# Kernel tuning notes

Measured on AMD Instinct MI355X. Metric: run time of the kernel, lower is better.

The kernel has to match this reference:

```python
import jax, jax.numpy as jnp
import numpy as np

B, N, IN_DIM, HID, OUT_DIM = 8, 1024, 768, 128, 768
H1, H2, MHA_HEADS, C = 8, 1, 4, 32
ALPHA = 0.2
NEG = -9e15
LN_EPS = 1e-5


def _gat_layer(x, W, a1, a2, adj_mask):
    # x: [B,N,Fin], W: [H,Fin,Fout], a1/a2: [H,Fout], adj_mask: [B,N,N] bool
    h = jnp.einsum('bni,hio->bhno', x, W)                      # [B,H,N,F]
    s1 = jnp.einsum('bhno,ho->bhn', h, a1)                     # score for source node i
    s2 = jnp.einsum('bhno,ho->bhn', h, a2)                     # score for target node j
    e = jax.nn.leaky_relu(s1[:, :, :, None] + s2[:, :, None, :], negative_slope=ALPHA)
    e = jnp.where(adj_mask[:, None, :, :], e, NEG)
    attn = jax.nn.softmax(e, axis=-1)                          # [B,H,N,N]
    hp = jnp.einsum('bhnm,bhmo->bhno', attn, h)                # [B,H,N,F]
    b, nh, n, f = hp.shape
    return hp.transpose(0, 2, 1, 3).reshape(b, n, nh * f)      # concat heads -> [B,N,H*F]


def _mha(q, k, v, wq, bq, wk, bk, wv, bv, wo, bo, n_heads):
    # torch-style MultiheadAttention (eval, no dropout). q:[B,Lq,E] k,v:[B,Lk,E]
    b, lq, e = q.shape
    lk = k.shape[1]
    hd = e // n_heads
    Q = (q @ wq + bq).reshape(b, lq, n_heads, hd).transpose(0, 2, 1, 3)
    K = (k @ wk + bk).reshape(b, lk, n_heads, hd).transpose(0, 2, 1, 3)
    V = (v @ wv + bv).reshape(b, lk, n_heads, hd).transpose(0, 2, 1, 3)
    scores = jnp.einsum('bhqd,bhkd->bhqk', Q, K) / jnp.sqrt(jnp.float32(hd))
    attn = jax.nn.softmax(scores, axis=-1)
    out = jnp.einsum('bhqk,bhkd->bhqd', attn, V)
    out = out.transpose(0, 2, 1, 3).reshape(b, lq, e)
    return out @ wo + bo


def _layernorm(x, g, b):
    mu = jnp.mean(x, axis=-1, keepdims=True)
    var = jnp.var(x, axis=-1, keepdims=True)
    return (x - mu) * jax.lax.rsqrt(var + LN_EPS) * g + b


def setup_inputs() -> dict:
    key = jax.random.key(0)
    ks = jax.random.split(key, 24)
    s = lambda fan_in: 1.0 / np.sqrt(fan_in)
    inp = {
        'node_features': jax.random.normal(ks[0], (B, N, IN_DIM), jnp.float32),
        'adjacency': jax.random.randint(ks[1], (B, N, N), 0, 2, jnp.int32),
        'context_indices': jax.random.randint(ks[2], (B, C), 0, N, jnp.int32),
        # GAT layer 1: 8 heads, in=768 -> out=128 each
        'W1': jax.random.normal(ks[3], (H1, IN_DIM, HID), jnp.float32) * s(IN_DIM),
        'a1_1': jax.random.normal(ks[4], (H1, HID), jnp.float32) * s(2 * HID),
        'a2_1': jax.random.normal(ks[5], (H1, HID), jnp.float32) * s(2 * HID),
        # GAT layer 2: 1 head, in=1024 -> out=128
        'W2': jax.random.normal(ks[6], (H2, HID * H1, HID), jnp.float32) * s(HID * H1),
        'a1_2': jax.random.normal(ks[7], (H2, HID), jnp.float32) * s(2 * HID),
        'a2_2': jax.random.normal(ks[8], (H2, HID), jnp.float32) * s(2 * HID),
        # query MultiheadAttention (embed_dim=128, 4 heads)
        'wq': jax.random.normal(ks[9], (HID, HID), jnp.float32) * s(HID),
        'bq': jnp.zeros((HID,), jnp.float32),
        'wk': jax.random.normal(ks[10], (HID, HID), jnp.float32) * s(HID),
        'bk': jnp.zeros((HID,), jnp.float32),
        'wv': jax.random.normal(ks[11], (HID, HID), jnp.float32) * s(HID),
        'bv': jnp.zeros((HID,), jnp.float32),
        'wo': jax.random.normal(ks[12], (HID, HID), jnp.float32) * s(HID),
        'bo': jnp.zeros((HID,), jnp.float32),
        # projection MLP
        'p1_w': jax.random.normal(ks[13], (HID, HID), jnp.float32) * s(HID),
        'p1_b': jnp.zeros((HID,), jnp.float32),
        'ln_g': jnp.ones((HID,), jnp.float32),
        'ln_b': jnp.zeros((HID,), jnp.float32),
        'p2_w': jax.random.normal(ks[14], (HID, OUT_DIM), jnp.float32) * s(HID),
        'p2_b': jnp.zeros((OUT_DIM,), jnp.float32),
    }
    return inp


def reference(node_features, adjacency, context_indices,
              W1, a1_1, a2_1, W2, a1_2, a2_2,
              wq, bq, wk, bk, wv, bv, wo, bo,
              p1_w, p1_b, ln_g, ln_b, p2_w, p2_b):
    adj_mask = adjacency > 0
    h = jax.nn.elu(_gat_layer(node_features, W1, a1_1, a2_1, adj_mask))  # [B,N,1024]
    h = jax.nn.elu(_gat_layer(h, W2, a1_2, a2_2, adj_mask))              # [B,N,128]
    q = h[:, 0:1, :]                                                      # [B,1,E]
    ctx = jnp.take_along_axis(h, context_indices[:, :, None], axis=1)     # [B,C,E]
    pooled = _mha(q, ctx, ctx, wq, bq, wk, bk, wv, bv, wo, bo, MHA_HEADS)[:, 0, :]
    z = jax.nn.relu(_layernorm(pooled @ p1_w + p1_b, ln_g, ln_b))
    return z @ p2_w + p2_b                                                # [B,OUT_DIM]
```

## Files before the change

### kernel.cpp

```cpp
#include <hip/hip_runtime.h>
#include <hip/hip_bf16.h>

#define ALPHA 0.2f
#define LOG2E 1.4426950408889634f

using short8  = __attribute__((ext_vector_type(8))) short;
using short4v = __attribute__((ext_vector_type(4))) short;
using f32x4   = __attribute__((ext_vector_type(4))) float;
using int4v   = __attribute__((ext_vector_type(4))) int;

static __device__ __forceinline__ float b2f(short s) {
    union { float f; unsigned u; } v; v.u = ((unsigned)(unsigned short)s) << 16; return v.f;
}
static __device__ __forceinline__ short f2bf(float f) {
    __hip_bfloat16 h = __float2bfloat16(f);
    return *reinterpret_cast<short*>(&h);
}
static __device__ __forceinline__ float fexp2(float x) {
    return __builtin_amdgcn_exp2f(x);
}
static __device__ __forceinline__ void gload_lds16(const void* g, void* l) {
    __builtin_amdgcn_global_load_lds(
        (const __attribute__((address_space(1))) unsigned*)g,
        (__attribute__((address_space(3))) unsigned*)l, 16, 0, 0);
}

__global__ __launch_bounds__(256) void k_prep(
        const int* __restrict__ adj, unsigned* __restrict__ adjb,
        const float* __restrict__ x, short* __restrict__ xb,
        const float* __restrict__ W1, short* __restrict__ W1T,
        const float* __restrict__ W2, short* __restrict__ W2T) {
    int bid = blockIdx.x, t = threadIdx.x;
    if (bid < 32768) {
        int idx = bid * 256 + t;
        int lane = t & 63;
        unsigned long long m = __ballot(adj[idx] > 0);
        if ((lane & 31) == 0) adjb[idx >> 5] = (unsigned)(m >> (lane & 32));
    } else if (bid < 38912) {
        int idx = (bid - 32768) * 256 + t;
        f32x4 v = ((const f32x4*)x)[idx];
        short4v o;
        o[0] = f2bf(v[0]); o[1] = f2bf(v[1]); o[2] = f2bf(v[2]); o[3] = f2bf(v[3]);
        ((short4v*)xb)[idx] = o;
    } else if (bid < 41984) {
        int idx = (bid - 38912) * 256 + t;
        int n = idx / 768, k = idx - n * 768;
        int h = n >> 7, o = n & 127;
        W1T[idx] = f2bf(W1[(h * 768 + k) * 128 + o]);
    } else {
        int idx = (bid - 41984) * 256 + t;
        int n = idx >> 10, k = idx & 1023;
        W2T[idx] = f2bf(W2[k * 128 + n]);
    }
}

__global__ __launch_bounds__(256) void k_gemm_bt(
        const short* __restrict__ A, const short* __restrict__ Bt,
        short* __restrict__ Ct, int K, int Ncols,
        const float* __restrict__ a1, const float* __restrict__ a2,
        float* __restrict__ s1, float* __restrict__ s2) {
    int tid = threadIdx.x, wave = tid >> 6, lane = tid & 63;
    int lr = lane & 15, lg = lane >> 4;
    int flat = blockIdx.y * gridDim.x + blockIdx.x;
    int chunkw = (gridDim.x * gridDim.y) >> 3;
    int swz = (flat & 7) * chunkw + (flat >> 3);
    int bx = swz % gridDim.x, by = swz / gridDim.x;
    int m0 = bx * 128, n0 = by * 128;
    int wm = (wave >> 1) * 64, wn = (wave & 1) * 64;
    __shared__ short lsA[2][128 * 64], lsB[2][128 * 64];
    __shared__ float sred1[2][128], sred2[2][128];
    f32x4 acc[4][4];
#pragma unroll
    for (int i = 0; i < 4; i++)
#pragma unroll
        for (int j = 0; j < 4; j++) acc[i][j] = (f32x4){0.f, 0.f, 0.f, 0.f};

    auto stage = [&](int bufsel, int k0) {
#pragma unroll
        for (int s = 0; s < 4; s++) {
            int chunk = s * 256 + tid;
            int r = chunk >> 3, c = chunk & 7;
            int csrc = c ^ (r & 7);
            gload_lds16(A + (size_t)(m0 + r) * K + k0 + csrc * 8, &lsA[bufsel][chunk * 8]);
            gload_lds16(Bt + (size_t)(n0 + r) * K + k0 + csrc * 8, &lsB[bufsel][chunk * 8]);
        }
    };
    auto compute = [&](const short* la, const short* lb) {
#pragma unroll
        for (int kk = 0; kk < 2; kk++) {
            short8 a[4], bb[4];
#pragma unroll
            for (int f = 0; f < 4; f++) {
                int ra = wm + f * 16 + lr, rb = wn + f * 16 + lr;
                a[f]  = *(const short8*)(la + ra * 64 + (((kk * 4 + lg) ^ (ra & 7)) * 8));
                bb[f] = *(const short8*)(lb + rb * 64 + (((kk * 4 + lg) ^ (rb & 7)) * 8));
            }
#pragma unroll
            for (int fm = 0; fm < 4; fm++)
#pragma unroll
                for (int fn = 0; fn < 4; fn++)
                    acc[fm][fn] = __builtin_amdgcn_mfma_f32_16x16x32_bf16(a[fm], bb[fn], acc[fm][fn], 0, 0, 0);
        }
    };
    stage(0, 0);
    __syncthreads();
    for (int k2 = 0; k2 < K; k2 += 128) {
        stage(1, k2 + 64);
        compute(lsA[0], lsB[0]);
        __syncthreads();
        if (k2 + 128 < K) stage(0, k2 + 128);
        compute(lsA[1], lsB[1]);
        __syncthreads();
    }
    short* stg = &lsA[0][0];
#pragma unroll
    for (int fm = 0; fm < 4; fm++) {
#pragma unroll
        for (int fn = 0; fn < 4; fn++) {
            int nl = wn + fn * 16 + lr;
            int i4w = (wm + fm * 16 + lg * 4) >> 2;
            short4v st;
            st[0] = f2bf(acc[fm][fn][0]); st[1] = f2bf(acc[fm][fn][1]);
            st[2] = f2bf(acc[fm][fn][2]); st[3] = f2bf(acc[fm][fn][3]);
            *(short4v*)(stg + (nl * 32 + (i4w ^ (nl & 31))) * 4) = st;
        }
    }
    __syncthreads();
    size_t gbase = ((size_t)(m0 >> 10) * Ncols + n0) * 1024 + (m0 & 1023);
#pragma unroll
    for (int it = 0; it < 8; it++) {
        int idx8 = it * 256 + tid;
        int nl = idx8 >> 4, p = idx8 & 15;
        int i4a = 2 * p, i4b = 2 * p + 1;
        short4v lo = *(short4v*)(stg + (nl * 32 + (i4a ^ (nl & 31))) * 4);
        short4v hi = *(short4v*)(stg + (nl * 32 + (i4b ^ (nl & 31))) * 4);
        short8 v;
#pragma unroll
        for (int r = 0; r < 4; r++) { v[r] = lo[r]; v[r + 4] = hi[r]; }
        *(short8*)(Ct + gbase + (size_t)nl * 1024 + p * 8) = v;
    }
    if (a1 != nullptr) {
        int h = by;
        float av1[4], av2[4];
#pragma unroll
        for (int fn = 0; fn < 4; fn++) {
            int o = wn + fn * 16 + lr;
            av1[fn] = a1[h * 128 + o];
            av2[fn] = a2[h * 128 + o];
        }
        int wcol = wave & 1;
#pragma unroll
        for (int fm = 0; fm < 4; fm++)
#pragma unroll
            for (int r = 0; r < 4; r++) {
                float v1 = acc[fm][0][r] * av1[0] + acc[fm][1][r] * av1[1]
                         + acc[fm][2][r] * av1[2] + acc[fm][3][r] * av1[3];
                float v2 = acc[fm][0][r] * av2[0] + acc[fm][1][r] * av2[1]
                         + acc[fm][2][r] * av2[2] + acc[fm][3][r] * av2[3];
#pragma unroll
                for (int off = 1; off < 16; off <<= 1) {
                    v1 += __shfl_xor(v1, off);
                    v2 += __shfl_xor(v2, off);
                }
                if (lr == 0) {
                    int il = wm + fm * 16 + lg * 4 + r;
                    sred1[wcol][il] = v1;
                    sred2[wcol][il] = v2;
                }
            }
        __syncthreads();
        if (tid < 128) {
            int b = m0 >> 10;
            int irow = (b * 8 + h) * 1024 + (m0 & 1023) + tid;
            s1[irow] = (sred1[0][tid] + sred1[1][tid]) * LOG2E;
            s2[irow] = (sred2[0][tid] + sred2[1][tid]) * LOG2E;
        }
    }
}

__global__ __launch_bounds__(256) void k_gemm64(
        const short* __restrict__ A, const short* __restrict__ Bt,
        short* __restrict__ Ct, int K, int Ncols) {
    int tid = threadIdx.x, wave = tid >> 6, lane = tid & 63;
    int lr = lane & 15, lg = lane >> 4;
    int flat = blockIdx.y * gridDim.x + blockIdx.x;
    int chunkw = (gridDim.x * gridDim.y) >> 3;
    int swz = (flat & 7) * chunkw + (flat >> 3);
    int bx = swz % gridDim.x, by = swz / gridDim.x;
    int m0 = bx * 64, n0 = by * 64;
    int wm = (wave >> 1) * 32, wn = (wave & 1) * 32;
    __shared__ short lsA[2][64 * 32], lsB[2][64 * 32];
    f32x4 acc[2][2];
#pragma unroll
    for (int i = 0; i < 2; i++)
#pragma unroll
        for (int j = 0; j < 2; j++) acc[i][j] = (f32x4){0.f, 0.f, 0.f, 0.f};

    auto stage = [&](int bufsel, int k0) {
        int r = tid >> 2, c = tid & 3;
        int csrc = c ^ (r & 3);
        int base = (wave * 64) * 8;
        gload_lds16(A + (size_t)(m0 + r) * K + k0 + csrc * 8, &lsA[bufsel][base]);
        gload_lds16(Bt + (size_t)(n0 + r) * K + k0 + csrc * 8, &lsB[bufsel][base]);
    };
    stage(0, 0);
    __syncthreads();
    int buf = 0;
    for (int k0 = 0; k0 < K; k0 += 32) {
        if (k0 + 32 < K) stage(buf ^ 1, k0 + 32);
        short8 a[2], bb[2];
#pragma unroll
        for (int f = 0; f < 2; f++) {
            int ra = wm + f * 16 + lr, rb = wn + f * 16 + lr;
            a[f]  = *(const short8*)(&lsA[buf][ra * 32 + ((lg ^ (ra & 3)) * 8)]);
            bb[f] = *(const short8*)(&lsB[buf][rb * 32 + ((lg ^ (rb & 3)) * 8)]);
        }
#pragma unroll
        for (int fm = 0; fm < 2; fm++)
#pragma unroll
            for (int fn = 0; fn < 2; fn++)
                acc[fm][fn] = __builtin_amdgcn_mfma_f32_16x16x32_bf16(a[fm], bb[fn], acc[fm][fn], 0, 0, 0);
        __syncthreads();
        buf ^= 1;
    }
#pragma unroll
    for (int fm = 0; fm < 2; fm++) {
        int mb = m0 + wm + fm * 16 + lg * 4;
        size_t obase = ((size_t)(mb >> 10) * Ncols) * 1024 + (mb & 1023);
#pragma unroll
        for (int fn = 0; fn < 2; fn++) {
            int n = n0 + wn + fn * 16 + lr;
            short4v st;
            st[0] = f2bf(acc[fm][fn][0]); st[1] = f2bf(acc[fm][fn][1]);
            st[2] = f2bf(acc[fm][fn][2]); st[3] = f2bf(acc[fm][fn][3]);
            *(short4v*)(Ct + obase + (size_t)n * 1024) = st;
        }
    }
}

__global__ __launch_bounds__(256) void k_s12(
        const short* __restrict__ ht, const float* __restrict__ a1,
        const float* __restrict__ a2, float* __restrict__ s1,
        float* __restrict__ s2, int nh) {
    int bh = blockIdx.x;
    int h = bh % nh;
    int i4 = threadIdx.x * 4;
    const short* base = ht + (size_t)bh * 131072 + i4;
    f32x4 acc1 = {0.f, 0.f, 0.f, 0.f}, acc2 = {0.f, 0.f, 0.f, 0.f};
#pragma unroll 8
    for (int o = 0; o < 128; o++) {
        short4v v = *(const short4v*)(base + ((size_t)o << 10));
        float w1 = a1[h * 128 + o], w2 = a2[h * 128 + o];
#pragma unroll
        for (int r = 0; r < 4; r++) {
            float f = b2f(v[r]);
            acc1[r] += f * w1;
            acc2[r] += f * w2;
        }
    }
#pragma unroll
    for (int r = 0; r < 4; r++) { acc1[r] *= LOG2E; acc2[r] *= LOG2E; }
    *(f32x4*)(s1 + bh * 1024 + i4) = acc1;
    *(f32x4*)(s2 + bh * 1024 + i4) = acc2;
}

__global__ __launch_bounds__(512) void k_attn1(
        const short* __restrict__ ht, const unsigned* __restrict__ adjb,
        const float* __restrict__ s1, const float* __restrict__ s2,
        short* __restrict__ out) {
    int flat = blockIdx.y * 8 + blockIdx.x;
    int swz = (flat & 7) * 64 + (flat >> 3);
    int bh = swz >> 3, bxi = swz & 7;
    int b = bh >> 3, h = bh & 7;
    int tid = threadIdx.x, wave = tid >> 6, lane = tid & 63;
    int lr = lane & 15, lg = lane >> 4;
    int ic = bxi * 128 + wave * 16 + lr;
    int row = bh * 1024 + ic;
    float s1i = s1[row];
    const unsigned long long* abrow =
        (const unsigned long long*)(adjb + ((size_t)(b << 10) + ic) * 32);
    const float* s2r = s2 + bh * 1024;
    const short* hbase = ht + (size_t)bh * 131072;

    __shared__ short lsh[2][16384];
    __shared__ float ls2[1024];
    f32x4 acc[8];
#pragma unroll
    for (int f = 0; f < 8; f++) acc[f] = (f32x4){0.f, 0.f, 0.f, 0.f};
    f32x4 accs = (f32x4){0.f, 0.f, 0.f, 0.f};
    short8 ones8;
#pragma unroll
    for (int e = 0; e < 8; e++) ones8[e] = (short)0x3F80;

    auto stage = [&](int bufsel, int j0) {
#pragma unroll
        for (int s = 0; s < 4; s++) {
            int chunk = s * 512 + tid;
            int r = chunk >> 4, c = chunk & 15;
            int csrc = c ^ (r & 15);
            gload_lds16(hbase + (size_t)r * 1024 + j0 + csrc * 8,
                        &lsh[bufsel][chunk * 8]);
        }
    };
    auto compute = [&](const short* ls, int j0) {
        unsigned long long aw0 = abrow[j0 >> 6], aw1 = abrow[(j0 >> 6) + 1];
#pragma unroll
        for (int kk = 0; kk < 4; kk++) {
            int jb = j0 + kk * 32 + lg * 8;
            f32x4 t0 = *(const f32x4*)(&ls2[jb]);
            f32x4 t1 = *(const f32x4*)(&ls2[jb + 4]);
            unsigned long long aw = (kk < 2) ? aw0 : aw1;
            unsigned bits = (unsigned)(aw >> ((kk & 1) * 32 + lg * 8)) & 0xFFu;
            float pv[8];
#pragma unroll
            for (int e = 0; e < 8; e++) {
                float sv = e < 4 ? t0[e] : t1[e & 3];
                float ee = s1i + sv;
                ee = fmaxf(ee, ALPHA * ee);
                float p = fexp2(ee);
                pv[e] = ((bits >> e) & 1) ? p : 0.f;
            }
            int4v pw;
#pragma unroll
            for (int w = 0; w < 4; w++) {
                int d;
                asm("v_cvt_pk_bf16_f32 %0, %1, %2"
                    : "=v"(d) : "v"(pv[2 * w]), "v"(pv[2 * w + 1]));
                pw[w] = d;
            }
            short8 pb = __builtin_bit_cast(short8, pw);
            __builtin_amdgcn_s_setprio(1);
            accs = __builtin_amdgcn_mfma_f32_16x16x32_bf16(ones8, pb, accs, 0, 0, 0);
#pragma unroll
            for (int fm = 0; fm < 8; fm++) {
                int r = fm * 16 + lr;
                int ck = (kk * 4 + lg) ^ (r & 15);
                short8 af = *(const short8*)(ls + r * 128 + ck * 8);
                acc[fm] = __builtin_amdgcn_mfma_f32_16x16x32_bf16(af, pb, acc[fm], 0, 0, 0);
            }
            __builtin_amdgcn_s_setprio(0);
        }
    };

    if (wave < 4) {
        gload_lds16(s2r + (wave * 64 + lane) * 4, &ls2[wave * 256]);
    }
    stage(0, 0);
    __syncthreads();
    for (int t2 = 0; t2 < 1024; t2 += 256) {
        stage(1, t2 + 128);
        compute(lsh[0], t2);
        __syncthreads();
        if (t2 + 256 < 1024) stage(0, t2 + 256);
        compute(lsh[1], t2 + 128);
        __syncthreads();
    }
    float rdi = 1.f / accs[0];
    size_t orow = ((size_t)(b << 10) + ic) * 1024 + h * 128;
#pragma unroll
    for (int fm = 0; fm < 8; fm++) {
        int ob = (fm << 4) + lg * 4;
        short4v st;
#pragma unroll
        for (int r = 0; r < 4; r++) {
            float x = acc[fm][r] * rdi;
            x = x > 0.f ? x : expm1f(x);
            st[r] = f2bf(x);
        }
        *(short4v*)(out + orow + ob) = st;
    }
}

__global__ __launch_bounds__(256) void k_attn2g(
        const short* __restrict__ h2t, const unsigned* __restrict__ adjb,
        const float* __restrict__ s1, const float* __restrict__ s2,
        const int* __restrict__ cidx, float* __restrict__ ghat) {
    int tile = blockIdx.x;
    int b = blockIdx.y;
    int tid = threadIdx.x, wave = tid >> 6, lane = tid & 63;
    int lr = lane & 15, lg = lane >> 4;

    __shared__ int nodes[16];
    __shared__ float sps[4][16];
    __shared__ float sacc[4][16][129];

    if (tid < 16) {
        int pos = tile * 16 + tid;
        int nd = 0;
        if (pos >= 1 && pos <= 32) nd = cidx[b * 32 + pos - 1];
        nodes[tid] = nd;
    }
    __syncthreads();

    const float* s2r = s2 + b * 1024;
    int nd = nodes[lr];
    float s1i = s1[b * 1024 + nd];
    const unsigned long long* abrow =
        (const unsigned long long*)(adjb + ((size_t)(b << 10) + nd) * 32);
    const short* hb = h2t + (size_t)b * 131072;
    f32x4 acc[8];
#pragma unroll
    for (int f = 0; f < 8; f++) acc[f] = (f32x4){0.f, 0.f, 0.f, 0.f};
    float psum = 0.f;

    for (int j0 = wave * 256; j0 < wave * 256 + 256; j0 += 32) {
        int jb = j0 + lg * 8;
        f32x4 t0 = *(const f32x4*)(s2r + jb);
        f32x4 t1 = *(const f32x4*)(s2r + jb + 4);
        unsigned bits = (unsigned)(abrow[j0 >> 6] >> ((j0 & 32) + lg * 8)) & 0xFFu;
        short8 pb;
#pragma unroll
        for (int e = 0; e < 8; e++) {
            float sv = e < 4 ? t0[e] : t1[e & 3];
            float ee = s1i + sv;
            ee = fmaxf(ee, ALPHA * ee);
            float p = fexp2(ee);
            p = ((bits >> e) & 1) ? p : 0.f;
            psum += p;
            pb[e] = f2bf(p);
        }
#pragma unroll
        for (int fm = 0; fm < 8; fm++) {
            short8 af = *(const short8*)(hb + (size_t)(fm * 16 + lr) * 1024 + jb);
            acc[fm] = __builtin_amdgcn_mfma_f32_16x16x32_bf16(af, pb, acc[fm], 0, 0, 0);
        }
    }
    psum += __shfl_xor(psum, 16);
    psum += __shfl_xor(psum, 32);
    if (lg == 0) sps[wave][lr] = psum;
#pragma unroll
    for (int fm = 0; fm < 8; fm++)
#pragma unroll
        for (int r = 0; r < 4; r++)
            sacc[wave][lr][fm * 16 + lg * 4 + r] = acc[fm][r];
    __syncthreads();
    for (int e = tid; e < 2048; e += 256) {
        int li = e >> 7, o = e & 127;
        float sum = sps[0][li] + sps[1][li] + sps[2][li] + sps[3][li];
        float v = (sacc[0][li][o] + sacc[1][li][o] + sacc[2][li][o] + sacc[3][li][o]) / sum;
        v = v > 0.f ? v : expm1f(v);
        ghat[((size_t)b * 48 + tile * 16 + li) * 128 + o] = v;
    }
}

__global__ __launch_bounds__(256) void k_qkv(
        const float* __restrict__ ghat,
        const float* __restrict__ wk, const float* __restrict__ bk,
        const float* __restrict__ wvp, const float* __restrict__ bv,
        float* __restrict__ Kp, float* __restrict__ Vp) {
    int b = blockIdx.y, rg = blockIdx.x & 7, o0 = (blockIdx.x >> 3) * 64;
    int t = threadIdx.x, wvi = t >> 6, ln = t & 63;
    __shared__ float sx[4][128];
    __shared__ float sWk[128 * 64], sWv[128 * 64];

    if (wvi < 2) {
        int cb = wvi * 64;
        gload_lds16(ghat + ((size_t)b * 48 + 1 + rg * 4) * 128 + (size_t)(cb + ln) * 4,
                    (float*)sx + cb * 4);
    }
#pragma unroll
    for (int s = 0; s < 8; s++) {
        int cb = s * 256 + wvi * 64;
        int q = cb + ln, rw = q >> 4, c4 = q & 15;
        gload_lds16(wk  + (size_t)rw * 128 + o0 + c4 * 4, &sWk[cb * 4]);
        gload_lds16(wvp + (size_t)rw * 128 + o0 + c4 * 4, &sWv[cb * 4]);
    }
    __syncthreads();
    int o = o0 + ln;
    float ka = bk[o], va = bv[o];
#pragma unroll 32
    for (int c = 0; c < 128; c++) {
        float x = sx[wvi][c];
        ka += x * sWk[c * 64 + ln];
        va += x * sWv[c * 64 + ln];
    }
    int r = rg * 4 + wvi;
    Kp[((size_t)b * 32 + r) * 128 + o] = ka;
    Vp[((size_t)b * 32 + r) * 128 + o] = va;
}

__global__ __launch_bounds__(256) void k_tail(
        const float* __restrict__ ghat, const float* __restrict__ Kp,
        const float* __restrict__ Vp,
        const float* __restrict__ wq, const float* __restrict__ bq,
        const float* __restrict__ wo, const float* __restrict__ bo,
        const float* __restrict__ p1w, const float* __restrict__ p1b,
        const float* __restrict__ lng, const float* __restrict__ lnb,
        float* __restrict__ tvec) {
    int b = blockIdx.x, t = threadIdx.x;
    int wvi = t >> 6, ln = t & 63;
    __shared__ float sq[128], sQ[128], sK[32][128], sV[32][128];
    __shared__ float sP[4][33], sO[128], sT[128], sZ[128];
    __shared__ float sred[2];
    __shared__ float sW[128 * 128];

#pragma unroll
    for (int s = 0; s < 4; s++) {
        int cb = s * 256 + wvi * 64;
        gload_lds16(Kp + (size_t)b * 4096 + (size_t)(cb + ln) * 4, (float*)sK + cb * 4);
        gload_lds16(Vp + (size_t)b * 4096 + (size_t)(cb + ln) * 4, (float*)sV + cb * 4);
    }
#pragma unroll
    for (int s = 0; s < 16; s++) {
        int cb = s * 256 + wvi * 64;
        gload_lds16(wq + (size_t)(cb + ln) * 4, &sW[cb * 4]);
    }
    if (t < 128) sq[t] = ghat[(size_t)b * 48 * 128 + t];
    __syncthreads();
    if (t < 128) {
        float a0 = 0.f, a1 = 0.f, a2 = 0.f, a3 = 0.f;
#pragma unroll
        for (int c = 0; c < 128; c += 4) {
            a0 += sq[c]     * sW[c * 128 + t];
            a1 += sq[c + 1] * sW[(c + 1) * 128 + t];
            a2 += sq[c + 2] * sW[(c + 2) * 128 + t];
            a3 += sq[c + 3] * sW[(c + 3) * 128 + t];
        }
        sQ[t] = bq[t] + ((a0 + a1) + (a2 + a3));
    }
    __syncthreads();
#pragma unroll
    for (int s = 0; s < 16; s++) {
        int cb = s * 256 + wvi * 64;
        gload_lds16(wo + (size_t)(cb + ln) * 4, &sW[cb * 4]);
    }
    if (t < 128) {
        int hh = t >> 5, jj = t & 31;
        float s = 0.f;
#pragma unroll
        for (int d = 0; d < 32; d++) s += sQ[hh * 32 + d] * sK[jj][hh * 32 + d];
        s *= 0.17677669529663687f;
        float m = s;
#pragma unroll
        for (int off = 16; off > 0; off >>= 1) m = fmaxf(m, __shfl_xor(m, off, 32));
        float p = __expf(s - m);
        float sum = p;
#pragma unroll
        for (int off = 16; off > 0; off >>= 1) sum += __shfl_xor(sum, off, 32);
        sP[hh][jj] = p / sum;
    }
    __syncthreads();
    if (t < 128) {
        int hh = t >> 5;
        float s = 0.f;
#pragma unroll
        for (int jj = 0; jj < 32; jj++) s += sP[hh][jj] * sV[jj][t];
        sO[t] = s;
    }
    __syncthreads();
    if (t < 128) {
        float a0 = 0.f, a1 = 0.f, a2 = 0.f, a3 = 0.f;
#pragma unroll
        for (int c = 0; c < 128; c += 4) {
            a0 += sO[c]     * sW[c * 128 + t];
            a1 += sO[c + 1] * sW[(c + 1) * 128 + t];
            a2 += sO[c + 2] * sW[(c + 2) * 128 + t];
            a3 += sO[c + 3] * sW[(c + 3) * 128 + t];
        }
        sT[t] = bo[t] + ((a0 + a1) + (a2 + a3));
    }
    __syncthreads();
#pragma unroll
    for (int s = 0; s < 16; s++) {
        int cb = s * 256 + wvi * 64;
        gload_lds16(p1w + (size_t)(cb + ln) * 4, &sW[cb * 4]);
    }
    __syncthreads();
    if (t < 128) {
        float a0 = 0.f, a1 = 0.f, a2 = 0.f, a3 = 0.f;
#pragma unroll
        for (int c = 0; c < 128; c += 4) {
            a0 += sT[c]     * sW[c * 128 + t];
            a1 += sT[c + 1] * sW[(c + 1) * 128 + t];
            a2 += sT[c + 2] * sW[(c + 2) * 128 + t];
            a3 += sT[c + 3] * sW[(c + 3) * 128 + t];
        }
        sZ[t] = p1b[t] + ((a0 + a1) + (a2 + a3));
    }
    __syncthreads();
    if (t < 64) {
        float v = sZ[t] + sZ[t + 64];
#pragma unroll
        for (int off = 32; off > 0; off >>= 1) v += __shfl_xor(v, off);
        if (t == 0) sred[0] = v * (1.f / 128.f);
    }
    __syncthreads();
    float mu = sred[0];
    if (t < 64) {
        float d1 = sZ[t] - mu, d2 = sZ[t + 64] - mu;
        float v = d1 * d1 + d2 * d2;
#pragma unroll
        for (int off = 32; off > 0; off >>= 1) v += __shfl_xor(v, off);
        if (t == 0) sred[1] = v * (1.f / 128.f);
    }
    __syncthreads();
    float rstd = rsqrtf(sred[1] + 1e-5f);
    if (t < 128) {
        float z = (sZ[t] - mu) * rstd * lng[t] + lnb[t];
        tvec[b * 128 + t] = fmaxf(z, 0.f);
    }
}

__global__ __launch_bounds__(256) void k_p2(
        const float* __restrict__ tvec, const float* __restrict__ p2w,
        const float* __restrict__ p2b, float* __restrict__ out) {
    int jj0 = blockIdx.x * 128, b = blockIdx.y;
    int t = threadIdx.x, wvi = t >> 6, ln = t & 63;
    __shared__ float sT[128];
    __shared__ float sW[128 * 128];

#pragma unroll
    for (int s = 0; s < 16; s++) {
        int cb = s * 256 + wvi * 64;
        int q = cb + ln, c = q >> 5, c4 = q & 31;
        gload_lds16(p2w + (size_t)c * 768 + jj0 + c4 * 4, &sW[cb * 4]);
    }
    if (t < 128) sT[t] = tvec[b * 128 + t];
    __syncthreads();
    if (t < 128) {
        float a0 = 0.f, a1 = 0.f, a2 = 0.f, a3 = 0.f;
#pragma unroll
        for (int c = 0; c < 128; c += 4) {
            a0 += sT[c]     * sW[c * 128 + t];
            a1 += sT[c + 1] * sW[(c + 1) * 128 + t];
            a2 += sT[c + 2] * sW[(c + 2) * 128 + t];
            a3 += sT[c + 3] * sW[(c + 3) * 128 + t];
        }
        out[b * 768 + jj0 + t] = p2b[jj0 + t] + ((a0 + a1) + (a2 + a3));
    }
}

extern "C" void kernel_launch(void* const* d_in, const int* in_sizes, int n_in,
                              void* d_out, int out_size, void* d_ws, size_t ws_size,
                              hipStream_t stream) {
    const float* x   = (const float*)d_in[0];
    const int*  adj  = (const int*)d_in[1];
    const int*  cidx = (const int*)d_in[2];
    const float* W1  = (const float*)d_in[3];
    const float* a11 = (const float*)d_in[4];
    const float* a21 = (const float*)d_in[5];
    const float* W2  = (const float*)d_in[6];
    const float* a12 = (const float*)d_in[7];
    const float* a22 = (const float*)d_in[8];
    const float* wq = (const float*)d_in[9];  const float* bq = (const float*)d_in[10];
    const float* wk = (const float*)d_in[11]; const float* bk = (const float*)d_in[12];
    const float* wv = (const float*)d_in[13]; const float* bv = (const float*)d_in[14];
    const float* wo = (const float*)d_in[15]; const float* bo = (const float*)d_in[16];
    const float* p1w = (const float*)d_in[17]; const float* p1b = (const float*)d_in[18];
    const float* lng = (const float*)d_in[19]; const float* lnb = (const float*)d_in[20];
    const float* p2w = (const float*)d_in[21]; const float* p2b = (const float*)d_in[22];
    float* out = (float*)d_out;

    char* ws = (char*)d_ws;
    size_t off = 0;
    auto alloc = [&](size_t bytes) -> char* {
        char* p = ws + off;
        off = (off + bytes + 255) & ~(size_t)255;
        return p;
    };
    short* Xb   = (short*)alloc(8192ull * 768 * 2);
    short* W1T  = (short*)alloc(1024ull * 768 * 2);
    short* W2T  = (short*)alloc(128ull * 1024 * 2);
    unsigned* adjb = (unsigned*)alloc(8ull * 1024 * 32 * 4);
    short* h1t  = (short*)alloc(64ull * 128 * 1024 * 2);
    float* s1a  = (float*)alloc(64ull * 1024 * 4);
    float* s2a  = (float*)alloc(64ull * 1024 * 4);
    short* hcat = (short*)alloc(8192ull * 1024 * 2);
    short* h2t  = (short*)alloc(8ull * 128 * 1024 * 2);
    float* s1b  = (float*)alloc(8192ull * 4);
    float* s2b  = (float*)alloc(8192ull * 4);
    float* ghat = (float*)alloc(8ull * 48 * 128 * 4);
    float* Kp   = (float*)alloc(8ull * 32 * 128 * 4);
    float* Vp   = (float*)alloc(8ull * 32 * 128 * 4);
    float* tvec = (float*)alloc(8ull * 128 * 4);
    if (off > ws_size) return;

    k_prep<<<42496, 256, 0, stream>>>(adj, adjb, x, Xb, W1, W1T, W2, W2T);

    k_gemm_bt<<<dim3(64, 8), 256, 0, stream>>>(Xb, W1T, h1t, 768, 1024,
                                               a11, a21, s1a, s2a);
    k_attn1<<<dim3(8, 64), 512, 0, stream>>>(h1t, adjb, s1a, s2a, hcat);

    k_gemm64<<<dim3(128, 2), 256, 0, stream>>>(hcat, W2T, h2t, 1024, 128);
    k_s12<<<8, 256, 0, stream>>>(h2t, a12, a22, s1b, s2b, 1);
    k_attn2g<<<dim3(3, 8), 256, 0, stream>>>(h2t, adjb, s1b, s2b, cidx, ghat);

    k_qkv<<<dim3(16, 8), 256, 0, stream>>>(ghat, wk, bk, wv, bv, Kp, Vp);
    k_tail<<<8, 256, 0, stream>>>(ghat, Kp, Vp, wq, bq, wo, bo,
                                  p1w, p1b, lng, lnb, tvec);
    k_p2<<<dim3(6, 8), 256, 0, stream>>>(tvec, p2w, p2b, out);
}
```

Measured before the change: 148.1 us.

## Switch GAT layer-1 attention to 32x32x16 MFMA with 32 rows per wave

Rewrites k_attn1 so each wave handles 32 query rows using the 32x32x16 bf16 MFMA instead of 16 rows with 16x16x32, halving the block to 256 threads. The softmax denominator is now a per-lane running sum plus a cross-half shuffle, replacing the extra ones-vector MFMA. The goal is to halve the exp/leaky-relu work per P element and reduce LDS fragment reads per MFMA. In exchange each block uses fewer waves and larger accumulator registers, and has to issue twice as many staging loads per thread.

```diff
diff --git a/kernel.cpp b/kernel.cpp
--- a/kernel.cpp
+++ b/kernel.cpp
@@ -7,6 +7,7 @@
 using short8  = __attribute__((ext_vector_type(8))) short;
 using short4v = __attribute__((ext_vector_type(4))) short;
 using f32x4   = __attribute__((ext_vector_type(4))) float;
+using f32x16  = __attribute__((ext_vector_type(16))) float;
 using int4v   = __attribute__((ext_vector_type(4))) int;
 
 static __device__ __forceinline__ float b2f(short s) {
@@ -264,7 +265,7 @@
     *(f32x4*)(s2 + bh * 1024 + i4) = acc2;
 }
 
-__global__ __launch_bounds__(512) void k_attn1(
+__global__ __launch_bounds__(256) void k_attn1(
         const short* __restrict__ ht, const unsigned* __restrict__ adjb,
         const float* __restrict__ s1, const float* __restrict__ s2,
         short* __restrict__ out) {
@@ -273,8 +274,8 @@
     int bh = swz >> 3, bxi = swz & 7;
     int b = bh >> 3, h = bh & 7;
     int tid = threadIdx.x, wave = tid >> 6, lane = tid & 63;
-    int lr = lane & 15, lg = lane >> 4;
-    int ic = bxi * 128 + wave * 16 + lr;
+    int li = lane & 31, jh = lane >> 5;
+    int ic = bxi * 128 + wave * 32 + li;
     int row = bh * 1024 + ic;
     float s1i = s1[row];
     const unsigned long long* abrow =
@@ -284,18 +285,17 @@
 
     __shared__ short lsh[2][16384];
     __shared__ float ls2[1024];
-    f32x4 acc[8];
-#pragma unroll
-    for (int f = 0; f < 8; f++) acc[f] = (f32x4){0.f, 0.f, 0.f, 0.f};
-    f32x4 accs = (f32x4){0.f, 0.f, 0.f, 0.f};
-    short8 ones8;
-#pragma unroll
-    for (int e = 0; e < 8; e++) ones8[e] = (short)0x3F80;
+    f32x16 acc[4];
+#pragma unroll
+    for (int f = 0; f < 4; f++)
+#pragma unroll
+        for (int r = 0; r < 16; r++) acc[f][r] = 0.f;
+    float psum = 0.f;
 
     auto stage = [&](int bufsel, int j0) {
 #pragma unroll
-        for (int s = 0; s < 4; s++) {
-            int chunk = s * 512 + tid;
+        for (int s = 0; s < 8; s++) {
+            int chunk = s * 256 + tid;
             int r = chunk >> 4, c = chunk & 15;
             int csrc = c ^ (r & 15);
             gload_lds16(hbase + (size_t)r * 1024 + j0 + csrc * 8,
@@ -303,14 +303,13 @@
         }
     };
     auto compute = [&](const short* ls, int j0) {
-        unsigned long long aw0 = abrow[j0 >> 6], aw1 = abrow[(j0 >> 6) + 1];
-#pragma unroll
-        for (int kk = 0; kk < 4; kk++) {
-            int jb = j0 + kk * 32 + lg * 8;
-            f32x4 t0 = *(const f32x4*)(&ls2[jb]);
-            f32x4 t1 = *(const f32x4*)(&ls2[jb + 4]);
-            unsigned long long aw = (kk < 2) ? aw0 : aw1;
-            unsigned bits = (unsigned)(aw >> ((kk & 1) * 32 + lg * 8)) & 0xFFu;
+#pragma unroll
+        for (int c16 = 0; c16 < 8; c16++) {
+            int jb = c16 * 16 + jh * 8;
+            int jg = j0 + jb;
+            f32x4 t0 = *(const f32x4*)(&ls2[jg]);
+            f32x4 t1 = *(const f32x4*)(&ls2[jg + 4]);
+            unsigned bits = (unsigned)(abrow[jg >> 6] >> (jg & 63)) & 0xFFu;
             float pv[8];
 #pragma unroll
             for (int e = 0; e < 8; e++) {
@@ -318,7 +317,9 @@
                 float ee = s1i + sv;
                 ee = fmaxf(ee, ALPHA * ee);
                 float p = fexp2(ee);
-                pv[e] = ((bits >> e) & 1) ? p : 0.f;
+                p = ((bits >> e) & 1) ? p : 0.f;
+                pv[e] = p;
+                psum += p;
             }
             int4v pw;
 #pragma unroll
@@ -329,22 +330,20 @@
                 pw[w] = d;
             }
             short8 pb = __builtin_bit_cast(short8, pw);
+            int cc = jb >> 3;
             __builtin_amdgcn_s_setprio(1);
-            accs = __builtin_amdgcn_mfma_f32_16x16x32_bf16(ones8, pb, accs, 0, 0, 0);
-#pragma unroll
-            for (int fm = 0; fm < 8; fm++) {
-                int r = fm * 16 + lr;
-                int ck = (kk * 4 + lg) ^ (r & 15);
+#pragma unroll
+            for (int ob = 0; ob < 4; ob++) {
+                int r = ob * 32 + li;
+                int ck = cc ^ (r & 15);
                 short8 af = *(const short8*)(ls + r * 128 + ck * 8);
-                acc[fm] = __builtin_amdgcn_mfma_f32_16x16x32_bf16(af, pb, acc[fm], 0, 0, 0);
+                acc[ob] = __builtin_amdgcn_mfma_f32_32x32x16_bf16(af, pb, acc[ob], 0, 0, 0);
             }
             __builtin_amdgcn_s_setprio(0);
         }
     };
 
-    if (wave < 4) {
-        gload_lds16(s2r + (wave * 64 + lane) * 4, &ls2[wave * 256]);
-    }
+    gload_lds16(s2r + (size_t)(wave * 64 + lane) * 4, &ls2[wave * 256]);
     stage(0, 0);
     __syncthreads();
     for (int t2 = 0; t2 < 1024; t2 += 256) {
@@ -355,19 +354,23 @@
         compute(lsh[1], t2 + 128);
         __syncthreads();
     }
-    float rdi = 1.f / accs[0];
+    psum += __shfl_xor(psum, 32);
+    float rdi = 1.f / psum;
     size_t orow = ((size_t)(b << 10) + ic) * 1024 + h * 128;
 #pragma unroll
-    for (int fm = 0; fm < 8; fm++) {
-        int ob = (fm << 4) + lg * 4;
-        short4v st;
-#pragma unroll
-        for (int r = 0; r < 4; r++) {
-            float x = acc[fm][r] * rdi;
-            x = x > 0.f ? x : expm1f(x);
-            st[r] = f2bf(x);
-        }
-        *(short4v*)(out + orow + ob) = st;
+    for (int ob = 0; ob < 4; ob++) {
+#pragma unroll
+        for (int q = 0; q < 4; q++) {
+            int m = 8 * q + 4 * jh;
+            short4v st;
+#pragma unroll
+            for (int r2 = 0; r2 < 4; r2++) {
+                float x = acc[ob][4 * q + r2] * rdi;
+                x = x > 0.f ? x : expm1f(x);
+                st[r2] = f2bf(x);
+            }
+            *(short4v*)(out + orow + ob * 32 + m) = st;
+        }
     }
 }
 
@@ -679,7 +682,7 @@
 
     k_gemm_bt<<<dim3(64, 8), 256, 0, stream>>>(Xb, W1T, h1t, 768, 1024,
                                                a11, a21, s1a, s2a);
-    k_attn1<<<dim3(8, 64), 512, 0, stream>>>(h1t, adjb, s1a, s2a, hcat);
+    k_attn1<<<dim3(8, 64), 256, 0, stream>>>(h1t, adjb, s1a, s2a, hcat);
 
     k_gemm64<<<dim3(128, 2), 256, 0, stream>>>(hcat, W2T, h2t, 1024, 128);
     k_s12<<<8, 256, 0, stream>>>(h2t, a12, a22, s1b, s2b, 1);
```

Result: slower. 155.6 us (+5.0%).
